# Optimization experiments

Hardware: AMD Instinct MI355X
Metric: run time of the kernel (lower is better)

The kernel has to match this reference:

```python
import jax, jax.numpy as jnp
import numpy as np

N_NODES = 100000
N_EDGES = 1600000
HIDDEN = 64
EDGE_DIM = 16


def setup_inputs() -> dict:
    key = jax.random.key(0)
    ks = jax.random.split(key, 9)
    x = jax.random.normal(ks[0], (N_NODES, HIDDEN), dtype=jnp.float32)
    edge_index = jax.random.randint(ks[1], (2, N_EDGES), 0, N_NODES, dtype=jnp.int32)
    edge_attr = jax.random.normal(ks[2], (N_EDGES, EDGE_DIM), dtype=jnp.float32)
    s1 = 1.0 / np.sqrt(HIDDEN * 2 + EDGE_DIM)
    s2 = 1.0 / np.sqrt(HIDDEN)
    s3 = 1.0 / np.sqrt(HIDDEN * 2)
    W1 = jax.random.uniform(ks[3], (HIDDEN * 2 + EDGE_DIM, HIDDEN), jnp.float32, -s1, s1)
    b1 = jax.random.uniform(ks[4], (HIDDEN,), jnp.float32, -s1, s1)
    W2 = jax.random.uniform(ks[5], (HIDDEN, HIDDEN), jnp.float32, -s2, s2)
    b2 = jax.random.uniform(ks[6], (HIDDEN,), jnp.float32, -s2, s2)
    W3 = jax.random.uniform(ks[7], (HIDDEN * 2, HIDDEN), jnp.float32, -s3, s3)
    b3 = jax.random.uniform(ks[8], (HIDDEN,), jnp.float32, -s3, s3)
    return {"x": x, "edge_index": edge_index, "edge_attr": edge_attr,
            "W1": W1, "b1": b1, "W2": W2, "b2": b2, "W3": W3, "b3": b3}


def reference(x, edge_index, edge_attr, W1, b1, W2, b2, W3, b3):
    src, dst = edge_index[0], edge_index[1]
    # edge MLP: Linear -> SiLU -> Linear -> SiLU
    m_in = jnp.concatenate([x[src], x[dst], edge_attr], axis=-1)  # [E, 2H+Ed]
    h = jax.nn.silu(m_in @ W1 + b1)
    messages = jax.nn.silu(h @ W2 + b2)  # [E, H]
    # scatter-add aggregate onto destination nodes
    agg = jax.ops.segment_sum(messages, dst, num_segments=x.shape[0])  # [N, H]
    # node MLP: Linear -> SiLU
    node_in = jnp.concatenate([x, agg], axis=-1)  # [N, 2H]
    return jax.nn.silu(node_in @ W3 + b3)
```

## Files before the change

kernel.cpp:

```cpp
#include <hip/hip_runtime.h>
#include <hip/hip_bf16.h>

#define NE 1600000
#define NN 100000
#define H 64
#define ED 16
#define NT (NE / 64)
#define NB1 391
#define NNB 1563

#define KS  72
#define K3S 136
#define YS  68

typedef __attribute__((ext_vector_type(8))) short short8;
typedef __attribute__((ext_vector_type(4))) float floatx4;

__device__ __forceinline__ unsigned short f2bf(float f) {
    union { float f; unsigned u; } v; v.f = f;
    unsigned r = v.u + 0x7fff + ((v.u >> 16) & 1);
    return (unsigned short)(r >> 16);
}

__device__ __forceinline__ float bf2f(unsigned short u) {
    union { unsigned u; float f; } v; v.u = ((unsigned)u) << 16;
    return v.f;
}

__device__ __forceinline__ unsigned cvt_pk_bf16(float lo, float hi) {
    unsigned r;
    asm("v_cvt_pk_bf16_f32 %0, %1, %2" : "=v"(r) : "v"(lo), "v"(hi));
    return r;
}

__device__ __forceinline__ float silu(float x) {
    return x * __builtin_amdgcn_rcpf(1.0f + __expf(-x));
}

__global__ void prep_kernel(const float* __restrict__ x,
                            const float* __restrict__ W1,
                            const float* __restrict__ b1,
                            const float* __restrict__ W2,
                            const float* __restrict__ W3,
                            const int* __restrict__ ei,
                            unsigned short* __restrict__ xb,
                            unsigned short* __restrict__ W1abT,
                            unsigned short* __restrict__ W1cT,
                            unsigned short* __restrict__ W2T,
                            unsigned short* __restrict__ W3T,
                            int* __restrict__ cnt) {
    int tid = blockIdx.x * blockDim.x + threadIdx.x;
    int nt = gridDim.x * blockDim.x;
    const float4* xv = (const float4*)x;
    uint2* xbv = (uint2*)xb;
    for (int i = tid; i < NN * H / 4; i += nt) {
        float4 v = xv[i];
        uint2 o;
        o.x = cvt_pk_bf16(v.x, v.y);
        o.y = cvt_pk_bf16(v.z, v.w);
        xbv[i] = o;
    }
    for (int i = tid; i < 128 * KS; i += nt) {
        int n = i / KS, k = i % KS;
        W1abT[i] = (k < 64) ? f2bf(W1[(size_t)((n < 64) ? k : 64 + k) * 64 + (n & 63)])
                            : (unsigned short)0;
    }
    for (int i = tid; i < 64 * 32; i += nt) {
        int n = i / 32, k = i % 32;
        unsigned short v = 0;
        if (k < 16) v = f2bf(W1[(size_t)(128 + k) * 64 + n]);
        else if (k == 16) v = f2bf(b1[n]);
        W1cT[i] = v;
    }
    for (int i = tid; i < 64 * KS; i += nt) {
        int n = i / KS, k = i % KS;
        W2T[i] = (k < 64) ? f2bf(W2[k * 64 + n]) : (unsigned short)0;
    }
    for (int i = tid; i < 64 * K3S; i += nt) {
        int n = i / K3S, k = i % K3S;
        W3T[i] = (k < 128) ? f2bf(W3[k * 64 + n]) : (unsigned short)0;
    }
    for (int e = tid; e < NE; e += nt) {
        atomicAdd(&cnt[ei[NE + e]], 1);
    }
}

__global__ void scan_block_kernel(const int* __restrict__ cnt,
                                  int* __restrict__ offs,
                                  int* __restrict__ bsums) {
    __shared__ int tmp[256];
    int b = blockIdx.x, i = threadIdx.x, idx = b * 256 + i;
    int v = (idx < NN) ? cnt[idx] : 0;
    tmp[i] = v;
    __syncthreads();
    #pragma unroll
    for (int off = 1; off < 256; off <<= 1) {
        int t2 = (i >= off) ? tmp[i - off] : 0;
        __syncthreads();
        tmp[i] += t2;
        __syncthreads();
    }
    if (idx < NN) offs[idx] = tmp[i] - v;
    if (i == 255) bsums[b] = tmp[255];
}

__global__ void scan_sums_kernel(int* __restrict__ bsums) {
    __shared__ int tmp[512];
    int i = threadIdx.x;
    int v = (i < NB1) ? bsums[i] : 0;
    tmp[i] = v;
    __syncthreads();
    #pragma unroll
    for (int off = 1; off < 512; off <<= 1) {
        int t2 = (i >= off) ? tmp[i - off] : 0;
        __syncthreads();
        tmp[i] += t2;
        __syncthreads();
    }
    if (i < NB1) bsums[i] = tmp[i] - v;
}

__global__ void scan_add_kernel(int* __restrict__ offs,
                                const int* __restrict__ bsums,
                                int* __restrict__ cursor) {
    int b = blockIdx.x, idx = b * 256 + threadIdx.x;
    if (idx < NN) {
        int o = offs[idx] + bsums[b];
        offs[idx] = o;
        cursor[idx] = o;
    }
}

__global__ void scatter_kernel(const int* __restrict__ ei,
                               int* __restrict__ cursor,
                               int4* __restrict__ sSDE) {
    int e = blockIdx.x * 256 + threadIdx.x;
    int src = ei[e], dst = ei[NE + e];
    int pos = atomicAdd(&cursor[dst], 1);
    int4 v; v.x = src; v.y = dst; v.z = e; v.w = 0;
    sSDE[pos] = v;
}

__global__ __launch_bounds__(256) void y12_kernel(
    const unsigned short* __restrict__ xb,
    const unsigned short* __restrict__ W1abT,
    unsigned short* __restrict__ yc) {
    __shared__ unsigned short sW[128 * KS];
    int t = threadIdx.x;
    {
        const uint4* wv = (const uint4*)W1abT;
        uint4* sv = (uint4*)sW;
        for (int i = t; i < 128 * KS * 2 / 16; i += 256) sv[i] = wv[i];
    }
    __syncthreads();

    int lane = t & 63, w = t >> 6;
    int m = lane & 15, q = lane >> 4;
    int n0 = blockIdx.x * 64;
    int node = n0 + w * 16 + m;
    int nclamp = (node < NN) ? node : (NN - 1);

    floatx4 acc[8];
    #pragma unroll
    for (int i = 0; i < 8; i++) acc[i] = (floatx4){0.f, 0.f, 0.f, 0.f};
    #pragma unroll
    for (int kt = 0; kt < 2; kt++) {
        short8 bfr = *(const short8*)(xb + (size_t)nclamp * H + kt * 32 + q * 8);
        #pragma unroll
        for (int tt = 0; tt < 8; tt++) {
            short8 afr = *(const short8*)(sW + (tt * 16 + m) * KS + kt * 32 + q * 8);
            acc[tt] = __builtin_amdgcn_mfma_f32_16x16x32_bf16(afr, bfr, acc[tt], 0, 0, 0);
        }
    }
    if (node < NN) {
        #pragma unroll
        for (int tt = 0; tt < 8; tt++) {
            uint2 o;
            o.x = cvt_pk_bf16(acc[tt][0], acc[tt][1]);
            o.y = cvt_pk_bf16(acc[tt][2], acc[tt][3]);
            *(uint2*)(yc + (size_t)node * 128 + tt * 16 + q * 4) = o;
        }
    }
}

__global__ __launch_bounds__(256, 6) void edge_kernel(
    const unsigned short* __restrict__ yc,
    const float* __restrict__ ea,
    const int4* __restrict__ sSDE,
    const unsigned short* __restrict__ W1cT,
    const unsigned short* __restrict__ W2T,
    const float* __restrict__ b2,
    float* __restrict__ agg) {
    __shared__ float sM[64 * YS];
    __shared__ unsigned short sH[64 * KS];
    __shared__ int sDst[64];

    int t = threadIdx.x;
    int lane = t & 63, w = t >> 6;
    int m = lane & 15, q = lane >> 4;
    int E = w * 16 + m;

    int4 sde = sSDE[(size_t)blockIdx.x * 64 + E];
    if (q == 0) sDst[E] = sde.y;
    int e = sde.z;

    union uf { unsigned u[4]; short8 s; };
    uf idA, idB;
    {
        unsigned val = (m & 1) ? 0x3F800000u : 0x00003F80u;
        int wsel = (m >> 1) & 3;
        bool gA = (q == (m >> 3));
        bool gB = (q == 2 + (m >> 3));
        #pragma unroll
        for (int i = 0; i < 4; i++) {
            idA.u[i] = (gA && wsel == i) ? val : 0u;
            idB.u[i] = (gB && wsel == i) ? val : 0u;
        }
    }

    short8 y1f0 = *(const short8*)(yc + (size_t)sde.x * 128 + q * 8);
    short8 y1f1 = *(const short8*)(yc + (size_t)sde.x * 128 + 32 + q * 8);
    short8 y2f0 = *(const short8*)(yc + (size_t)sde.y * 128 + 64 + q * 8);
    short8 y2f1 = *(const short8*)(yc + (size_t)sde.y * 128 + 96 + q * 8);

    short8 bf1 = {0, 0, 0, 0, 0, 0, 0, 0};
    if (q < 2) {
        const float4* p = (const float4*)(ea + (size_t)e * ED + q * 8);
        float4 v0 = p[0], v1 = p[1];
        union { unsigned u[4]; short8 s; } ub;
        ub.u[0] = cvt_pk_bf16(v0.x, v0.y);
        ub.u[1] = cvt_pk_bf16(v0.z, v0.w);
        ub.u[2] = cvt_pk_bf16(v1.x, v1.y);
        ub.u[3] = cvt_pk_bf16(v1.z, v1.w);
        bf1 = ub.s;
    } else if (q == 2) {
        bf1[0] = (short)0x3F80;
    }

    floatx4 acc[4];
    #pragma unroll
    for (int tt = 0; tt < 4; tt++) {
        short8 w1c = *(const short8*)(W1cT + (tt * 16 + m) * 32 + q * 8);
        floatx4 a = (floatx4){0.f, 0.f, 0.f, 0.f};
        a = __builtin_amdgcn_mfma_f32_16x16x32_bf16(w1c, bf1, a, 0, 0, 0);
        short8 idt = (tt & 1) ? idB.s : idA.s;
        a = __builtin_amdgcn_mfma_f32_16x16x32_bf16(idt, (tt >> 1) ? y1f1 : y1f0, a, 0, 0, 0);
        a = __builtin_amdgcn_mfma_f32_16x16x32_bf16(idt, (tt >> 1) ? y2f1 : y2f0, a, 0, 0, 0);
        acc[tt] = a;
    }

    #pragma unroll
    for (int tt = 0; tt < 4; tt++) {
        uint2 hp;
        hp.x = cvt_pk_bf16(silu(acc[tt][0]), silu(acc[tt][1]));
        hp.y = cvt_pk_bf16(silu(acc[tt][2]), silu(acc[tt][3]));
        *(uint2*)(sH + E * KS + tt * 16 + q * 4) = hp;
    }

    floatx4 acc2[4];
    #pragma unroll
    for (int i = 0; i < 4; i++) acc2[i] = (floatx4){0.f, 0.f, 0.f, 0.f};
    #pragma unroll
    for (int kt = 0; kt < 2; kt++) {
        short8 hfr = *(const short8*)(sH + E * KS + kt * 32 + q * 8);
        #pragma unroll
        for (int tt = 0; tt < 4; tt++) {
            short8 w2 = *(const short8*)(W2T + (tt * 16 + m) * KS + kt * 32 + q * 8);
            acc2[tt] = __builtin_amdgcn_mfma_f32_16x16x32_bf16(w2, hfr, acc2[tt], 0, 0, 0);
        }
    }

    #pragma unroll
    for (int tt = 0; tt < 4; tt++) {
        float4 bb = *(const float4*)(b2 + tt * 16 + q * 4);
        float4 mv;
        mv.x = silu(acc2[tt][0] + bb.x);
        mv.y = silu(acc2[tt][1] + bb.y);
        mv.z = silu(acc2[tt][2] + bb.z);
        mv.w = silu(acc2[tt][3] + bb.w);
        *(float4*)(sM + E * YS + tt * 16 + q * 4) = mv;
    }

    {
        int c = lane;
        float s = 0.f;
        int cur = sDst[w * 16];
        #pragma unroll
        for (int r = 0; r < 16; r++) {
            int rr = w * 16 + r;
            int d = sDst[rr];
            if (d != cur) {
                atomicAdd(&agg[(size_t)cur * H + c], s);
                s = 0.f;
                cur = d;
            }
            s += sM[rr * YS + c];
        }
        atomicAdd(&agg[(size_t)cur * H + c], s);
    }
}

__global__ __launch_bounds__(256) void node_kernel(
    const unsigned short* __restrict__ xb,
    const float* __restrict__ agg,
    const unsigned short* __restrict__ W3T,
    const float* __restrict__ b3,
    float* __restrict__ out) {
    __shared__ unsigned short sW3[64 * K3S];
    __shared__ unsigned short sA[64 * K3S];

    int t = threadIdx.x;
    int n0 = blockIdx.x * 64;

    {
        const uint4* wv = (const uint4*)W3T;
        uint4* sv = (uint4*)sW3;
        for (int i = t; i < 64 * K3S * 2 / 16; i += 256) sv[i] = wv[i];
    }
    {
        int nL = t >> 2, sub = t & 3;
        int node = n0 + nL;
        uint4* arow = (uint4*)(sA + nL * K3S);
        if (node < NN) {
            const uint4* xs = (const uint4*)(xb + (size_t)node * H);
            arow[sub * 2]     = xs[sub * 2];
            arow[sub * 2 + 1] = xs[sub * 2 + 1];
            const float4* av = (const float4*)(agg + (size_t)node * H);
            unsigned tmp[8];
            #pragma unroll
            for (int j = 0; j < 4; j++) {
                float4 v = av[sub * 4 + j];
                tmp[j * 2 + 0] = cvt_pk_bf16(v.x, v.y);
                tmp[j * 2 + 1] = cvt_pk_bf16(v.z, v.w);
            }
            uint4* drow = (uint4*)(sA + nL * K3S + 64 + sub * 16);
            drow[0] = ((const uint4*)tmp)[0];
            drow[1] = ((const uint4*)tmp)[1];
        } else {
            uint4 z = {0, 0, 0, 0};
            arow[sub * 2] = z; arow[sub * 2 + 1] = z;
            uint4* drow = (uint4*)(sA + nL * K3S + 64 + sub * 16);
            drow[0] = z; drow[1] = z;
        }
    }
    __syncthreads();

    int w = t >> 6, lane = t & 63;
    int m = lane & 15, q = lane >> 4;
    int node = n0 + w * 16 + m;

    floatx4 acc[4];
    #pragma unroll
    for (int i = 0; i < 4; i++) acc[i] = (floatx4){0.f, 0.f, 0.f, 0.f};
    #pragma unroll
    for (int kt = 0; kt < 4; kt++) {
        short8 bfr = *(const short8*)(sA + (w * 16 + m) * K3S + kt * 32 + q * 8);
        #pragma unroll
        for (int tt = 0; tt < 4; tt++) {
            short8 afr = *(const short8*)(sW3 + (tt * 16 + m) * K3S + kt * 32 + q * 8);
            acc[tt] = __builtin_amdgcn_mfma_f32_16x16x32_bf16(afr, bfr, acc[tt], 0, 0, 0);
        }
    }
    if (node < NN) {
        #pragma unroll
        for (int tt = 0; tt < 4; tt++) {
            float4 bb = *(const float4*)(b3 + tt * 16 + q * 4);
            float4 ov;
            ov.x = silu(acc[tt][0] + bb.x);
            ov.y = silu(acc[tt][1] + bb.y);
            ov.z = silu(acc[tt][2] + bb.z);
            ov.w = silu(acc[tt][3] + bb.w);
            *(float4*)(out + (size_t)node * H + tt * 16 + q * 4) = ov;
        }
    }
}

static inline size_t align256(size_t x) { return (x + 255) & ~(size_t)255; }

extern "C" void kernel_launch(void* const* d_in, const int* in_sizes, int n_in,
                              void* d_out, int out_size, void* d_ws, size_t ws_size,
                              hipStream_t stream) {
    const float* x  = (const float*)d_in[0];
    const int*   ei = (const int*)d_in[1];
    const float* ea = (const float*)d_in[2];
    const float* W1 = (const float*)d_in[3];
    const float* b1 = (const float*)d_in[4];
    const float* W2 = (const float*)d_in[5];
    const float* b2 = (const float*)d_in[6];
    const float* W3 = (const float*)d_in[7];
    const float* b3 = (const float*)d_in[8];
    float* out = (float*)d_out;

    char* ws = (char*)d_ws;
    size_t o = 0;
    float* agg = (float*)(ws + o);                    o = align256(o + (size_t)NN * H * 4);
    unsigned short* xb = (unsigned short*)(ws + o);   o = align256(o + (size_t)NN * H * 2);
    unsigned short* yc = (unsigned short*)(ws + o);   o = align256(o + (size_t)NN * 128 * 2);
    unsigned short* W1abT = (unsigned short*)(ws + o); o = align256(o + 128 * KS * 2);
    unsigned short* W1cT = (unsigned short*)(ws + o); o = align256(o + 64 * 32 * 2);
    unsigned short* W2T = (unsigned short*)(ws + o);  o = align256(o + 64 * KS * 2);
    unsigned short* W3T = (unsigned short*)(ws + o);  o = align256(o + 64 * K3S * 2);
    int* offs = (int*)(ws + o);                       o = align256(o + (size_t)NN * 4);
    int* bsums = (int*)(ws + o);                      o = align256(o + NB1 * 4);
    int* cnt = (int*)(ws + o);                        o = align256(o + (size_t)NN * 4);
    int4* sSDE = (int4*)(ws + o);                     o = align256(o + (size_t)NE * 16);

    int* cursor = cnt;

    hipMemsetAsync(agg, 0, (size_t)NN * H * sizeof(float), stream);
    hipMemsetAsync(cnt, 0, (size_t)NN * sizeof(int), stream);
    prep_kernel<<<2048, 256, 0, stream>>>(x, W1, b1, W2, W3, ei, xb, W1abT, W1cT, W2T, W3T, cnt);
    scan_block_kernel<<<NB1, 256, 0, stream>>>(cnt, offs, bsums);
    scan_sums_kernel<<<1, 512, 0, stream>>>(bsums);
    scan_add_kernel<<<NB1, 256, 0, stream>>>(offs, bsums, cursor);
    scatter_kernel<<<NE / 256, 256, 0, stream>>>(ei, cursor, sSDE);
    y12_kernel<<<NNB, 256, 0, stream>>>(xb, W1abT, yc);
    edge_kernel<<<NT, 256, 0, stream>>>(yc, ea, sSDE, W1cT, W2T, b2, agg);
    node_kernel<<<NNB, 256, 0, stream>>>(xb, agg, W3T, b3, out);
}
```

Before: 521.8 us.

## Pack sorted edge records into 64-bit words and alias per-wave shared buffers

Edge records (src, dst, edge id) are bit-packed into a single 64-bit word instead of an int4, halving scatter writes and edge-kernel index reads. The hidden and message shared-memory buffers are merged into one per-wave region, cutting LDS use so occupancy hints can rise from 6 to 8 blocks. The agg zeroing moves into the prep kernel, replacing a separate memset. Packing relies on node and edge counts fitting in 17 and 30 bits.

```diff
diff --git a/kernel.cpp b/kernel.cpp
--- a/kernel.cpp
+++ b/kernel.cpp
@@ -48,7 +48,8 @@
                             unsigned short* __restrict__ W1cT,
                             unsigned short* __restrict__ W2T,
                             unsigned short* __restrict__ W3T,
-                            int* __restrict__ cnt) {
+                            int* __restrict__ cnt,
+                            float4* __restrict__ aggv) {
     int tid = blockIdx.x * blockDim.x + threadIdx.x;
     int nt = gridDim.x * blockDim.x;
     const float4* xv = (const float4*)x;
@@ -60,6 +61,10 @@
         o.y = cvt_pk_bf16(v.z, v.w);
         xbv[i] = o;
     }
+    {
+        float4 z = {0.f, 0.f, 0.f, 0.f};
+        for (int i = tid; i < NN * H / 4; i += nt) aggv[i] = z;
+    }
     for (int i = tid; i < 128 * KS; i += nt) {
         int n = i / KS, k = i % KS;
         W1abT[i] = (k < 64) ? f2bf(W1[(size_t)((n < 64) ? k : 64 + k) * 64 + (n & 63)])
@@ -133,11 +138,13 @@
 
 __global__ void scatter_kernel(const int* __restrict__ ei,
                                int* __restrict__ cursor,
-                               int4* __restrict__ sSDE) {
+                               unsigned long long* __restrict__ sSDE) {
     int e = blockIdx.x * 256 + threadIdx.x;
     int src = ei[e], dst = ei[NE + e];
     int pos = atomicAdd(&cursor[dst], 1);
-    int4 v; v.x = src; v.y = dst; v.z = e; v.w = 0;
+    unsigned long long v = (unsigned long long)src
+                         | ((unsigned long long)dst << 17)
+                         | ((unsigned long long)e << 34);
     sSDE[pos] = v;
 }
 
@@ -183,16 +190,15 @@
     }
 }
 
-__global__ __launch_bounds__(256, 6) void edge_kernel(
+__global__ __launch_bounds__(256, 8) void edge_kernel(
     const unsigned short* __restrict__ yc,
     const float* __restrict__ ea,
-    const int4* __restrict__ sSDE,
+    const unsigned long long* __restrict__ sSDE,
     const unsigned short* __restrict__ W1cT,
     const unsigned short* __restrict__ W2T,
     const float* __restrict__ b2,
     float* __restrict__ agg) {
-    __shared__ float sM[64 * YS];
-    __shared__ unsigned short sH[64 * KS];
+    __shared__ float sWS[4][1088];
     __shared__ int sDst[64];
 
     int t = threadIdx.x;
@@ -200,9 +206,11 @@
     int m = lane & 15, q = lane >> 4;
     int E = w * 16 + m;
 
-    int4 sde = sSDE[(size_t)blockIdx.x * 64 + E];
-    if (q == 0) sDst[E] = sde.y;
-    int e = sde.z;
+    unsigned long long sde = sSDE[(size_t)blockIdx.x * 64 + E];
+    int src = (int)(sde & 0x1FFFF);
+    int dst = (int)((sde >> 17) & 0x1FFFF);
+    int e   = (int)(sde >> 34);
+    if (q == 0) sDst[E] = dst;
 
     union uf { unsigned u[4]; short8 s; };
     uf idA, idB;
@@ -218,10 +226,10 @@
         }
     }
 
-    short8 y1f0 = *(const short8*)(yc + (size_t)sde.x * 128 + q * 8);
-    short8 y1f1 = *(const short8*)(yc + (size_t)sde.x * 128 + 32 + q * 8);
-    short8 y2f0 = *(const short8*)(yc + (size_t)sde.y * 128 + 64 + q * 8);
-    short8 y2f1 = *(const short8*)(yc + (size_t)sde.y * 128 + 96 + q * 8);
+    short8 y1f0 = *(const short8*)(yc + (size_t)src * 128 + q * 8);
+    short8 y1f1 = *(const short8*)(yc + (size_t)src * 128 + 32 + q * 8);
+    short8 y2f0 = *(const short8*)(yc + (size_t)dst * 128 + 64 + q * 8);
+    short8 y2f1 = *(const short8*)(yc + (size_t)dst * 128 + 96 + q * 8);
 
     short8 bf1 = {0, 0, 0, 0, 0, 0, 0, 0};
     if (q < 2) {
@@ -249,12 +257,13 @@
         acc[tt] = a;
     }
 
+    unsigned short* sHw = (unsigned short*)sWS[w];
     #pragma unroll
     for (int tt = 0; tt < 4; tt++) {
         uint2 hp;
         hp.x = cvt_pk_bf16(silu(acc[tt][0]), silu(acc[tt][1]));
         hp.y = cvt_pk_bf16(silu(acc[tt][2]), silu(acc[tt][3]));
-        *(uint2*)(sH + E * KS + tt * 16 + q * 4) = hp;
+        *(uint2*)(sHw + m * KS + tt * 16 + q * 4) = hp;
     }
 
     floatx4 acc2[4];
@@ -262,7 +271,7 @@
     for (int i = 0; i < 4; i++) acc2[i] = (floatx4){0.f, 0.f, 0.f, 0.f};
     #pragma unroll
     for (int kt = 0; kt < 2; kt++) {
-        short8 hfr = *(const short8*)(sH + E * KS + kt * 32 + q * 8);
+        short8 hfr = *(const short8*)(sHw + m * KS + kt * 32 + q * 8);
         #pragma unroll
         for (int tt = 0; tt < 4; tt++) {
             short8 w2 = *(const short8*)(W2T + (tt * 16 + m) * KS + kt * 32 + q * 8);
@@ -270,6 +279,7 @@
         }
     }
 
+    float* sMw = sWS[w];
     #pragma unroll
     for (int tt = 0; tt < 4; tt++) {
         float4 bb = *(const float4*)(b2 + tt * 16 + q * 4);
@@ -278,7 +288,7 @@
         mv.y = silu(acc2[tt][1] + bb.y);
         mv.z = silu(acc2[tt][2] + bb.z);
         mv.w = silu(acc2[tt][3] + bb.w);
-        *(float4*)(sM + E * YS + tt * 16 + q * 4) = mv;
+        *(float4*)(sMw + m * YS + tt * 16 + q * 4) = mv;
     }
 
     {
@@ -287,14 +297,13 @@
         int cur = sDst[w * 16];
         #pragma unroll
         for (int r = 0; r < 16; r++) {
-            int rr = w * 16 + r;
-            int d = sDst[rr];
+            int d = sDst[w * 16 + r];
             if (d != cur) {
                 atomicAdd(&agg[(size_t)cur * H + c], s);
                 s = 0.f;
                 cur = d;
             }
-            s += sM[rr * YS + c];
+            s += sMw[r * YS + c];
         }
         atomicAdd(&agg[(size_t)cur * H + c], s);
     }
@@ -403,13 +412,13 @@
     int* offs = (int*)(ws + o);                       o = align256(o + (size_t)NN * 4);
     int* bsums = (int*)(ws + o);                      o = align256(o + NB1 * 4);
     int* cnt = (int*)(ws + o);                        o = align256(o + (size_t)NN * 4);
-    int4* sSDE = (int4*)(ws + o);                     o = align256(o + (size_t)NE * 16);
+    unsigned long long* sSDE = (unsigned long long*)(ws + o); o = align256(o + (size_t)NE * 8);
 
     int* cursor = cnt;
 
-    hipMemsetAsync(agg, 0, (size_t)NN * H * sizeof(float), stream);
     hipMemsetAsync(cnt, 0, (size_t)NN * sizeof(int), stream);
-    prep_kernel<<<2048, 256, 0, stream>>>(x, W1, b1, W2, W3, ei, xb, W1abT, W1cT, W2T, W3T, cnt);
+    prep_kernel<<<2048, 256, 0, stream>>>(x, W1, b1, W2, W3, ei, xb, W1abT, W1cT, W2T, W3T,
+                                          cnt, (float4*)agg);
     scan_block_kernel<<<NB1, 256, 0, stream>>>(cnt, offs, bsums);
     scan_sums_kernel<<<1, 512, 0, stream>>>(bsums);
     scan_add_kernel<<<NB1, 256, 0, stream>>>(offs, bsums, cursor);
```

Result: faster. 510.0 us (-2.3%).
